# Performance work log

Hardware: AMD Instinct MI355X
Metric: run time of the kernel (lower is better)

The kernel has to match this reference:

```python
import jax, jax.numpy as jnp
import numpy as np

N_FREQ = 7  # freqs = 2**linspace(0, 6, 7) == 2**arange(7)
SKIP = (4,)


def nerf_encode(p):
    # nerfstudio NeRFEncoding with include_input=True, windows_param=None
    freqs = 2.0 ** jnp.arange(N_FREQ, dtype=p.dtype)          # [7]
    scaled = (2.0 * jnp.pi) * p                               # [N,3]
    s = (scaled[..., None] * freqs).reshape(p.shape[0], -1)   # [N,21]
    enc = jnp.sin(jnp.concatenate([s, s + 0.5 * jnp.pi], axis=-1))  # [N,42] = sin | cos
    return jnp.concatenate([enc, p], axis=-1)                 # [N,45]


def _hat_pt3d(w):
    # pytorch3d hat convention (transpose of the standard skew matrix)
    x, y, z = w[:, 0], w[:, 1], w[:, 2]
    o = jnp.zeros_like(x)
    return jnp.stack([
        jnp.stack([o, z, -y], -1),
        jnp.stack([-z, o, x], -1),
        jnp.stack([y, -x, o], -1)], -2)                       # [N,3,3]


def se3_exp_map_T(screw, eps=1e-4):
    # pytorch3d.transforms.se3_exp_map(screw).permute(0, 2, 1)
    v, w = screw[:, :3], screw[:, 3:]
    ang2 = jnp.clip(jnp.sum(w * w, axis=-1), eps, None)
    ang = jnp.sqrt(ang2)
    K = _hat_pt3d(w)
    KK = jnp.matmul(K, K)
    f1 = (jnp.sin(ang) / ang)[:, None, None]
    f2 = ((1.0 - jnp.cos(ang)) / ang2)[:, None, None]
    f3 = ((ang - jnp.sin(ang)) / (ang * ang2))[:, None, None]
    I = jnp.eye(3, dtype=screw.dtype)
    R = I + f1 * K + f2 * KK       # pytorch3d (row-vector) rotation
    V = I + f2 * K + f3 * KK
    T = jnp.einsum('nij,nj->ni', V, v)
    M = jnp.zeros((screw.shape[0], 4, 4), screw.dtype)
    M = M.at[:, :3, :3].set(jnp.swapaxes(R, -1, -2))  # transpose of [[R,0],[T,1]]
    M = M.at[:, :3, 3].set(T)
    M = M.at[:, 3, 3].set(1.0)
    return M


def mlp_stem(x, Ws, bs):
    inp = x
    n = len(Ws)
    for i in range(n):
        if i in SKIP:
            x = jnp.concatenate([inp, x], axis=-1)
        x = x @ Ws[i].T + bs[i]
        x = jax.nn.relu(x)  # hidden activation; i==n-1 is out_activation (also ReLU)
    return x


def setup_inputs() -> dict:
    key = jax.random.key(0)
    ks = jax.random.split(key, 16)
    N = 524288
    d = {
        'positions': jax.random.uniform(ks[0], (N, 3), jnp.float32),
        'directions': jax.random.normal(ks[1], (N, 3), jnp.float32),
        'warp_code': jax.random.normal(ks[2], (N, 8), jnp.float32),
    }
    fan_ins = [53, 128, 128, 128, 181, 128]
    for i, fi in enumerate(fan_ins):
        d[f'W{i}'] = jax.random.normal(ks[3 + i], (128, fi), jnp.float32) / np.sqrt(fi)
        d[f'b{i}'] = jnp.zeros((128,), jnp.float32)
    d['Wr'] = jax.random.normal(ks[10], (3, 128), jnp.float32) * 1e-5
    d['br'] = jnp.zeros((3,), jnp.float32)
    d['Wv'] = jax.random.normal(ks[11], (3, 128), jnp.float32) * 1e-5
    d['bv'] = jnp.zeros((3,), jnp.float32)
    return d


def reference(positions, directions, warp_code,
              W0, b0, W1, b1, W2, b2, W3, b3, W4, b4, W5, b5,
              Wr, br, Wv, bv):
    enc = nerf_encode(positions)                                  # [N,45]
    feat = mlp_stem(jnp.concatenate([enc, warp_code], axis=-1),
                    [W0, W1, W2, W3, W4, W5], [b0, b1, b2, b3, b4, b5])  # [N,128]
    r = feat @ Wr.T + br                                          # [N,3]
    v = feat @ Wv.T + bv                                          # [N,3]
    screw = jnp.concatenate([v, r], axis=-1)                      # [N,6]
    M = se3_exp_map_T(screw)                                      # [N,4,4]
    ph = jnp.concatenate([positions, jnp.ones_like(positions[:, :1])], axis=-1)
    wp_h = jnp.einsum('nij,nj->ni', M, ph)                        # [N,4]
    wp = wp_h[:, :3] / wp_h[:, 3:]
    wp = jnp.where(jnp.isnan(wp), positions, wp)
    rots = M[:, :3, :3]
    wd = jnp.einsum('nij,nj->ni', rots, directions)
    wd = jnp.where(jnp.isnan(wd), directions, wd)
    return wp, wd
```

## Files before the change

### kernel.cpp

```cpp
#include <hip/hip_runtime.h>
#include <hip/hip_bf16.h>
#include <math.h>


typedef __bf16 bf16x8 __attribute__((ext_vector_type(8)));
typedef float  f32x4  __attribute__((ext_vector_type(4)));

#define NROWS 524288
#define BROWS 128

#define P0 0
#define P1 8192
#define P2 24576
#define P3 40960
#define P4 57344
#define P5 81920
#define PH 98304
#define PTOT 100352

#define X0_OFF 0
#define XA_OFF 16384
#define SC_OFF 0
#define LDS_SZ 49152

template<int KS, int FAN>
__device__ __forceinline__ float pack_val(const float* __restrict__ W, int idx)
{
    int f  = idx / (KS * 512);
    int r2 = idx % (KS * 512);
    int s  = r2 >> 9, r3 = r2 & 511, ln = r3 >> 3, j = r3 & 7;
    int col = f * 16 + (ln & 15);
    int k   = s * 32 + (ln >> 4) * 8 + j;
    if (FAN == 128) return W[col * 128 + k];
    if (FAN == 53)  return (k < 53) ? W[col * 53 + k] : 0.f;
    if (k < 53)  return W[col * 181 + k];
    if (k < 64)  return 0.f;
    return W[col * 181 + (k - 11)];
}

__global__ void pack_w(const float* __restrict__ W0, const float* __restrict__ W1,
                       const float* __restrict__ W2, const float* __restrict__ W3,
                       const float* __restrict__ W4, const float* __restrict__ W5,
                       const float* __restrict__ Wr, const float* __restrict__ Wv,
                       __bf16* __restrict__ pk)
{
    int e = blockIdx.x * 256 + threadIdx.x;
    if (e >= PTOT) return;
    float val;
    if (e >= PH) {
        int rem = e - PH;
        int s = rem >> 9, r3 = rem & 511, ln = r3 >> 3, j = r3 & 7;
        int col = ln & 15;
        int k = s * 32 + (ln >> 4) * 8 + j;
        if (col < 3)      val = Wv[col * 128 + k];
        else if (col < 6) val = Wr[(col - 3) * 128 + k];
        else              val = 0.f;
    }
    else if (e < P1) val = pack_val<2, 53 >(W0, e - P0);
    else if (e < P2) val = pack_val<4, 128>(W1, e - P1);
    else if (e < P3) val = pack_val<4, 128>(W2, e - P2);
    else if (e < P4) val = pack_val<4, 128>(W3, e - P3);
    else if (e < P5) val = pack_val<6, 181>(W4, e - P4);
    else             val = pack_val<4, 128>(W5, e - P5);
    pk[e] = (__bf16)val;
}

__device__ __forceinline__ unsigned pack_bf16_2(float a, float b) {
    union { __bf16 h; unsigned short u; } x, y;
    x.h = (__bf16)a; y.h = (__bf16)b;
    return ((unsigned)y.u << 16) | (unsigned)x.u;
}

template<int KS, int SPLITS, int KSN>
__device__ __forceinline__ void mlp_layer(unsigned char* smem,
    bf16x8 (&W)[4][4], f32x4 (&Bias)[4],
    const __bf16* __restrict__ pkCur, const __bf16* __restrict__ pkNext,
    const float* __restrict__ biasNext,
    int inOff, int inStride, int outOff,
    int lane, int cl, int gp, int mfG, int nfG)
{
    f32x4 acc[4][4];
    #pragma unroll
    for (int mf = 0; mf < 4; mf++)
        #pragma unroll
        for (int nf = 0; nf < 4; nf++) acc[mf][nf] = Bias[mf];

    bf16x8 Bf[2][4];
    auto loadB = [&](bf16x8* dst, int s) {
        int base, stride, k0;
        if (s < SPLITS) { base = X0_OFF; stride = 128;      k0 = s * 32; }
        else            { base = inOff;  stride = inStride; k0 = (s - SPLITS) * 32; }
        int bc = 2 * k0 + 16 * gp;
        #pragma unroll
        for (int nf = 0; nf < 4; nf++) {
            int row = nfG * 64 + nf * 16 + cl;
            dst[nf] = *(const bf16x8*)(smem + base + row * stride
                                       + (bc ^ ((row & 7) << 4)));
        }
    };

    loadB(Bf[0], 0);
    #pragma unroll
    for (int s = 0; s < KS; s++) {
        if (s + 1 < KS) loadB(Bf[(s + 1) & 1], s + 1);
        #pragma unroll
        for (int mf = 0; mf < 4; mf++)
            #pragma unroll
            for (int nf = 0; nf < 4; nf++)
                acc[mf][nf] = __builtin_amdgcn_mfma_f32_16x16x32_bf16(
                    W[s & 3][mf], Bf[s & 1][nf], acc[mf][nf], 0, 0, 0);
        if constexpr (KS > 4) {
            if (s + 4 < KS) {
                const bf16x8* pC = (const bf16x8*)pkCur;
                #pragma unroll
                for (int mf = 0; mf < 4; mf++)
                    W[(s + 4) & 3][mf] = pC[((mfG * 4 + mf) * KS + (s + 4)) * 64 + lane];
            }
        }
    }

    __syncthreads();

    if constexpr (KSN > 0) {
        constexpr int PF = (KSN > 4) ? 4 : KSN;
        const bf16x8* pN = (const bf16x8*)pkNext;
        #pragma unroll
        for (int s = 0; s < PF; s++)
            #pragma unroll
            for (int mf = 0; mf < 4; mf++)
                W[s][mf] = pN[((mfG * 4 + mf) * KSN + s) * 64 + lane];
        #pragma unroll
        for (int mf = 0; mf < 4; mf++)
            Bias[mf] = *(const f32x4*)(biasNext + mfG * 64 + mf * 16 + gp * 4);
    }

    #pragma unroll
    for (int mf = 0; mf < 4; mf++)
        #pragma unroll
        for (int nf = 0; nf < 4; nf++) {
            int row = nfG * 64 + nf * 16 + cl;
            int bc  = 128 * mfG + 32 * mf + 8 * gp;
            f32x4 a = acc[mf][nf];
            uint2 w;
            w.x = pack_bf16_2(fmaxf(a[0], 0.f), fmaxf(a[1], 0.f));
            w.y = pack_bf16_2(fmaxf(a[2], 0.f), fmaxf(a[3], 0.f));
            *(uint2*)(smem + outOff + row * 256 + (bc ^ ((row & 7) << 4))) = w;
        }

    asm volatile("s_waitcnt lgkmcnt(0)" ::: "memory");
    __builtin_amdgcn_s_barrier();
    asm volatile("" ::: "memory");
}

__global__ __launch_bounds__(256, 3)
void se3_fused(const float* __restrict__ pos, const float* __restrict__ dir,
               const float* __restrict__ wcode,
               const float* __restrict__ b0, const float* __restrict__ b1,
               const float* __restrict__ b2, const float* __restrict__ b3,
               const float* __restrict__ b4, const float* __restrict__ b5,
               const float* __restrict__ br, const float* __restrict__ bv,
               const __bf16* __restrict__ pk,
               float* __restrict__ out)
{
    __shared__ unsigned char smem[LDS_SZ];
    const int tid  = threadIdx.x;
    const int lane = tid & 63;
    const int cl   = lane & 15;
    const int gp   = lane >> 4;
    const int wid  = tid >> 6;
    const int mfG  = wid & 1;
    const int nfG  = wid >> 1;
    const int r0   = blockIdx.x * BROWS;

    bf16x8 W[4][4];
    f32x4  Bias[4];
    {
        const bf16x8* p0v = (const bf16x8*)(pk + P0);
        #pragma unroll
        for (int s = 0; s < 2; s++)
            #pragma unroll
            for (int mf = 0; mf < 4; mf++)
                W[s][mf] = p0v[((mfG * 4 + mf) * 2 + s) * 64 + lane];
        #pragma unroll
        for (int mf = 0; mf < 4; mf++)
            Bias[mf] = *(const f32x4*)(b0 + mfG * 64 + mf * 16 + gp * 4);
    }

    {
        int row = tid >> 1, h = tid & 1;
        int g = r0 + row;
        float p0 = pos[g*3+0], p1 = pos[g*3+1], p2 = pos[g*3+2];
        float vals[32];
        if (h == 0) {
            #pragma unroll
            for (int j = 0; j < 21; j++) {
                float p = (j < 7) ? p0 : (j < 14 ? p1 : p2);
                float t = p * (float)(1 << (j % 7));
                t -= floorf(t);
                vals[j] = __sinf(6.283185307179586f * t);
            }
            #pragma unroll
            for (int j = 21; j < 32; j++) {
                int idx = j - 21;
                float p = (idx < 7) ? p0 : (idx < 14 ? p1 : p2);
                float t = p * (float)(1 << (idx % 7));
                t -= floorf(t);
                vals[j] = __cosf(6.283185307179586f * t);
            }
        } else {
            #pragma unroll
            for (int j = 0; j < 10; j++) {
                int idx = 11 + j;
                float p = (idx < 14) ? p1 : p2;
                float t = p * (float)(1 << (idx % 7));
                t -= floorf(t);
                vals[j] = __cosf(6.283185307179586f * t);
            }
            vals[10] = p0; vals[11] = p1; vals[12] = p2;
            const float4* wc4 = (const float4*)(wcode + (size_t)g * 8);
            float4 wa = wc4[0], wb = wc4[1];
            vals[13] = wa.x; vals[14] = wa.y; vals[15] = wa.z; vals[16] = wa.w;
            vals[17] = wb.x; vals[18] = wb.y; vals[19] = wb.z; vals[20] = wb.w;
            #pragma unroll
            for (int j = 21; j < 32; j++) vals[j] = 0.f;
        }
        unsigned pkd[16];
        #pragma unroll
        for (int i = 0; i < 16; i++) pkd[i] = pack_bf16_2(vals[2*i], vals[2*i+1]);
        unsigned char* base = smem + X0_OFF + row * 128;
        int sw = (row & 7) << 4;
        #pragma unroll
        for (int c = 0; c < 4; c++) {
            uint4 w; w.x = pkd[4*c]; w.y = pkd[4*c+1]; w.z = pkd[4*c+2]; w.w = pkd[4*c+3];
            *(uint4*)(base + ((64 * h + 16 * c) ^ sw)) = w;
        }
    }
    __syncthreads();

    mlp_layer<2,0,4>(smem, W, Bias, pk+P0, pk+P1, b1, X0_OFF, 128, XA_OFF, lane, cl, gp, mfG, nfG);
    mlp_layer<4,0,4>(smem, W, Bias, pk+P1, pk+P2, b2, XA_OFF, 256, XA_OFF, lane, cl, gp, mfG, nfG);
    mlp_layer<4,0,4>(smem, W, Bias, pk+P2, pk+P3, b3, XA_OFF, 256, XA_OFF, lane, cl, gp, mfG, nfG);
    mlp_layer<4,0,6>(smem, W, Bias, pk+P3, pk+P4, b4, XA_OFF, 256, XA_OFF, lane, cl, gp, mfG, nfG);
    mlp_layer<6,2,4>(smem, W, Bias, pk+P4, pk+P5, b5, XA_OFF, 256, XA_OFF, lane, cl, gp, mfG, nfG);
    mlp_layer<4,0,0>(smem, W, Bias, pk+P5, nullptr, nullptr, XA_OFF, 256, XA_OFF, lane, cl, gp, mfG, nfG);

    if (mfG == 0) {
        const bf16x8* pW = (const bf16x8*)(pk + PH);
        bf16x8 Wh[4];
        #pragma unroll
        for (int s = 0; s < 4; s++) Wh[s] = pW[s * 64 + lane];
        f32x4 hb;
        #pragma unroll
        for (int r = 0; r < 4; r++) {
            int m = gp * 4 + r;
            hb[r] = (m < 3) ? bv[m] : ((m < 6) ? br[m - 3] : 0.f);
        }
        f32x4 hacc[4];
        #pragma unroll
        for (int nf = 0; nf < 4; nf++) hacc[nf] = hb;
        #pragma unroll
        for (int s = 0; s < 4; s++) {
            int bc = 64 * s + 16 * gp;
            #pragma unroll
            for (int nf = 0; nf < 4; nf++) {
                int row = nfG * 64 + nf * 16 + cl;
                bf16x8 B = *(const bf16x8*)(smem + XA_OFF + row * 256
                                            + (bc ^ ((row & 7) << 4)));
                hacc[nf] = __builtin_amdgcn_mfma_f32_16x16x32_bf16(Wh[s], B, hacc[nf], 0, 0, 0);
            }
        }
        #pragma unroll
        for (int nf = 0; nf < 4; nf++) {
            int row = nfG * 64 + nf * 16 + cl;
            if (gp == 0) {
                *(f32x4*)(smem + SC_OFF + row * 32) = hacc[nf];
            } else if (gp == 1) {
                *(float*)(smem + SC_OFF + row * 32 + 16) = hacc[nf][0];
                *(float*)(smem + SC_OFF + row * 32 + 20) = hacc[nf][1];
            }
        }
    }
    __syncthreads();

    if (tid < BROWS) {
        int row = tid, g = r0 + row;
        const float* sc = (const float*)(smem + SC_OFF + row * 32);
        float v0 = sc[0], v1 = sc[1], v2 = sc[2];
        float wx = sc[3], wy = sc[4], wz = sc[5];
        float ang2 = wx*wx + wy*wy + wz*wz;
        ang2 = fmaxf(ang2, 1e-4f);
        float ang = sqrtf(ang2);
        float sn = __sinf(ang), cs = __cosf(ang);
        float f1 = sn / ang;
        float f2 = (1.f - cs) / ang2;
        float f3 = (ang - sn) / (ang * ang2);
        float K[3][3] = {{0.f,  wz, -wy}, {-wz, 0.f,  wx}, { wy, -wx, 0.f}};
        float KK[3][3];
        #pragma unroll
        for (int i = 0; i < 3; i++)
            #pragma unroll
            for (int j = 0; j < 3; j++)
                KK[i][j] = K[i][0]*K[0][j] + K[i][1]*K[1][j] + K[i][2]*K[2][j];
        float R[3][3], V[3][3];
        #pragma unroll
        for (int i = 0; i < 3; i++)
            #pragma unroll
            for (int j = 0; j < 3; j++) {
                float id = (i == j) ? 1.f : 0.f;
                R[i][j] = id + f1 * K[i][j] + f2 * KK[i][j];
                V[i][j] = id + f2 * K[i][j] + f3 * KK[i][j];
            }
        float T0 = V[0][0]*v0 + V[0][1]*v1 + V[0][2]*v2;
        float T1 = V[1][0]*v0 + V[1][1]*v1 + V[1][2]*v2;
        float T2 = V[2][0]*v0 + V[2][1]*v1 + V[2][2]*v2;
        float px = pos[g*3+0], py = pos[g*3+1], pz = pos[g*3+2];
        float dx = dir[g*3+0], dy = dir[g*3+1], dz = dir[g*3+2];
        float wpx = R[0][0]*px + R[1][0]*py + R[2][0]*pz + T0;
        float wpy = R[0][1]*px + R[1][1]*py + R[2][1]*pz + T1;
        float wpz = R[0][2]*px + R[1][2]*py + R[2][2]*pz + T2;
        float wdx = R[0][0]*dx + R[1][0]*dy + R[2][0]*dz;
        float wdy = R[0][1]*dx + R[1][1]*dy + R[2][1]*dz;
        float wdz = R[0][2]*dx + R[1][2]*dy + R[2][2]*dz;
        wpx = (wpx != wpx) ? px : wpx;
        wpy = (wpy != wpy) ? py : wpy;
        wpz = (wpz != wpz) ? pz : wpz;
        wdx = (wdx != wdx) ? dx : wdx;
        wdy = (wdy != wdy) ? dy : wdy;
        wdz = (wdz != wdz) ? dz : wdz;
        out[g*3+0] = wpx; out[g*3+1] = wpy; out[g*3+2] = wpz;
        float* o2 = out + (size_t)NROWS * 3;
        o2[g*3+0] = wdx; o2[g*3+1] = wdy; o2[g*3+2] = wdz;
    }
}

extern "C" void kernel_launch(void* const* d_in, const int* in_sizes, int n_in,
                              void* d_out, int out_size, void* d_ws, size_t ws_size,
                              hipStream_t stream)
{
    const float* pos = (const float*)d_in[0];
    const float* dir = (const float*)d_in[1];
    const float* wc  = (const float*)d_in[2];
    const float* W0 = (const float*)d_in[3];  const float* b0 = (const float*)d_in[4];
    const float* W1 = (const float*)d_in[5];  const float* b1 = (const float*)d_in[6];
    const float* W2 = (const float*)d_in[7];  const float* b2 = (const float*)d_in[8];
    const float* W3 = (const float*)d_in[9];  const float* b3 = (const float*)d_in[10];
    const float* W4 = (const float*)d_in[11]; const float* b4 = (const float*)d_in[12];
    const float* W5 = (const float*)d_in[13]; const float* b5 = (const float*)d_in[14];
    const float* Wr = (const float*)d_in[15]; const float* br = (const float*)d_in[16];
    const float* Wv = (const float*)d_in[17]; const float* bv = (const float*)d_in[18];
    __bf16* pk = (__bf16*)d_ws;
    float* out = (float*)d_out;

    pack_w<<<(PTOT + 255) / 256, 256, 0, stream>>>(W0, W1, W2, W3, W4, W5, Wr, Wv, pk);
    se3_fused<<<NROWS / BROWS, 256, 0, stream>>>(pos, dir, wc,
                                                 b0, b1, b2, b3, b4, b5,
                                                 br, bv, pk, out);
}
```

Baseline: 224.7 us.

## Keep MLP activations in registers and stage weights through double-buffered LDS

Each block now handles 512 rows with 8 waves. Each wave owns 64 rows and computes all 128 output features. Hidden activations stay in registers across layers and are rearranged into the next layer's B-operand layout with cross-lane shuffles, so the per-layer LDS write/read round-trip goes away. Weights and biases for the next layer are copied into a second LDS buffer with global_load_lds while the current layer runs, replacing per-wave global weight fetches into registers. The trade is about 150 KB of LDS per block, which likely limits each CU to one block, and relies on the async LDS loads being complete by the barrier.

```diff
diff --git a/kernel.cpp b/kernel.cpp
--- a/kernel.cpp
+++ b/kernel.cpp
@@ -5,9 +5,10 @@
 
 typedef __bf16 bf16x8 __attribute__((ext_vector_type(8)));
 typedef float  f32x4  __attribute__((ext_vector_type(4)));
+typedef unsigned uintx4 __attribute__((ext_vector_type(4)));
 
 #define NROWS 524288
-#define BROWS 128
+#define BROWS 512
 
 #define P0 0
 #define P1 8192
@@ -18,10 +19,12 @@
 #define PH 98304
 #define PTOT 100352
 
-#define X0_OFF 0
-#define XA_OFF 16384
-#define SC_OFF 0
-#define LDS_SZ 49152
+#define WA_OFF   0
+#define WB_OFF   49152
+#define X0_OFF   81920
+#define BIAS_OFF 147456
+#define SCREW_OFF 49152
+#define LDS_SZ   150784
 
 template<int KS, int FAN>
 __device__ __forceinline__ float pack_val(const float* __restrict__ W, int idx)
@@ -71,88 +74,88 @@
     return ((unsigned)y.u << 16) | (unsigned)x.u;
 }
 
-template<int KS, int SPLITS, int KSN>
-__device__ __forceinline__ void mlp_layer(unsigned char* smem,
-    bf16x8 (&W)[4][4], f32x4 (&Bias)[4],
-    const __bf16* __restrict__ pkCur, const __bf16* __restrict__ pkNext,
-    const float* __restrict__ biasNext,
-    int inOff, int inStride, int outOff,
-    int lane, int cl, int gp, int mfG, int nfG)
-{
-    f32x4 acc[4][4];
+__device__ __forceinline__ void gload_lds16(const __bf16* g, unsigned char* l) {
+    __builtin_amdgcn_global_load_lds(
+        (const __attribute__((address_space(1))) unsigned int*)g,
+        (__attribute__((address_space(3))) unsigned int*)l, 16, 0, 0);
+}
+
+__device__ __forceinline__ void stageW(const __bf16* __restrict__ pkL,
+                                       unsigned char* wdst, int nfrags,
+                                       int w, int lane) {
+    for (int f = w; f < nfrags; f += 8)
+        gload_lds16(pkL + f * 512 + lane * 8, wdst + f * 1024);
+}
+
+template<int KS, int SPLIT>
+__device__ __forceinline__ void layer16(
+    unsigned char* smem, int wOff, int lyr,
+    const __bf16* __restrict__ pkNext, int nFragsNext, int wOffNext,
+    uintx4 (&X)[4][4],
+    int w, int lane, int c, int g, int sA, int sB, int hiG)
+{
+    f32x4 acc[8][4];
     #pragma unroll
-    for (int mf = 0; mf < 4; mf++)
-        #pragma unroll
-        for (int nf = 0; nf < 4; nf++) acc[mf][nf] = Bias[mf];
-
-    bf16x8 Bf[2][4];
-    auto loadB = [&](bf16x8* dst, int s) {
-        int base, stride, k0;
-        if (s < SPLITS) { base = X0_OFF; stride = 128;      k0 = s * 32; }
-        else            { base = inOff;  stride = inStride; k0 = (s - SPLITS) * 32; }
-        int bc = 2 * k0 + 16 * gp;
-        #pragma unroll
-        for (int nf = 0; nf < 4; nf++) {
-            int row = nfG * 64 + nf * 16 + cl;
-            dst[nf] = *(const bf16x8*)(smem + base + row * stride
-                                       + (bc ^ ((row & 7) << 4)));
-        }
-    };
-
-    loadB(Bf[0], 0);
+    for (int mf = 0; mf < 8; mf++) {
+        f32x4 bb = *(const f32x4*)(smem + BIAS_OFF + (lyr * 128 + mf * 16 + g * 4) * 4);
+        #pragma unroll
+        for (int nf = 0; nf < 4; nf++) acc[mf][nf] = bb;
+    }
+
+    stageW(pkNext, smem + wOffNext, nFragsNext, w, lane);
+
     #pragma unroll
     for (int s = 0; s < KS; s++) {
-        if (s + 1 < KS) loadB(Bf[(s + 1) & 1], s + 1);
-        #pragma unroll
-        for (int mf = 0; mf < 4; mf++)
+        bf16x8 Bf[4];
+        #pragma unroll
+        for (int nf = 0; nf < 4; nf++) {
+            if (s < SPLIT) {
+                int row = 64 * w + nf * 16 + c;
+                Bf[nf] = *(const bf16x8*)(smem + X0_OFF + row * 128
+                                          + ((64 * s + 16 * g) ^ ((row & 7) << 4)));
+            } else {
+                Bf[nf] = __builtin_bit_cast(bf16x8, X[(s >= SPLIT) ? s - SPLIT : 0][nf]);
+            }
+        }
+        #pragma unroll
+        for (int mf = 0; mf < 8; mf++) {
+            bf16x8 Wf = *(const bf16x8*)(smem + wOff + (mf * KS + s) * 1024 + lane * 16);
             #pragma unroll
             for (int nf = 0; nf < 4; nf++)
                 acc[mf][nf] = __builtin_amdgcn_mfma_f32_16x16x32_bf16(
-                    W[s & 3][mf], Bf[s & 1][nf], acc[mf][nf], 0, 0, 0);
-        if constexpr (KS > 4) {
-            if (s + 4 < KS) {
-                const bf16x8* pC = (const bf16x8*)pkCur;
-                #pragma unroll
-                for (int mf = 0; mf < 4; mf++)
-                    W[(s + 4) & 3][mf] = pC[((mfG * 4 + mf) * KS + (s + 4)) * 64 + lane];
-            }
-        }
-    }
-
+                    Wf, Bf[nf], acc[mf][nf], 0, 0, 0);
+        }
+    }
+
+    #pragma unroll
+    for (int nf = 0; nf < 4; nf++) {
+        unsigned lo[8], hi[8];
+        #pragma unroll
+        for (int mf = 0; mf < 8; mf++) {
+            f32x4 a = acc[mf][nf];
+            lo[mf] = pack_bf16_2(fmaxf(a[0], 0.f), fmaxf(a[1], 0.f));
+            hi[mf] = pack_bf16_2(fmaxf(a[2], 0.f), fmaxf(a[3], 0.f));
+        }
+        #pragma unroll
+        for (int s = 0; s < 4; s++) {
+            unsigned e0 = (unsigned)__shfl((int)lo[2*s],   sA, 64);
+            unsigned e1 = (unsigned)__shfl((int)lo[2*s+1], sA, 64);
+            unsigned f0 = (unsigned)__shfl((int)hi[2*s],   sA, 64);
+            unsigned f1 = (unsigned)__shfl((int)hi[2*s+1], sA, 64);
+            unsigned e2 = (unsigned)__shfl((int)lo[2*s],   sB, 64);
+            unsigned e3 = (unsigned)__shfl((int)lo[2*s+1], sB, 64);
+            unsigned f2 = (unsigned)__shfl((int)hi[2*s],   sB, 64);
+            unsigned f3 = (unsigned)__shfl((int)hi[2*s+1], sB, 64);
+            X[s][nf][0] = hiG ? e1 : e0;
+            X[s][nf][1] = hiG ? f1 : f0;
+            X[s][nf][2] = hiG ? e3 : e2;
+            X[s][nf][3] = hiG ? f3 : f2;
+        }
+    }
     __syncthreads();
-
-    if constexpr (KSN > 0) {
-        constexpr int PF = (KSN > 4) ? 4 : KSN;
-        const bf16x8* pN = (const bf16x8*)pkNext;
-        #pragma unroll
-        for (int s = 0; s < PF; s++)
-            #pragma unroll
-            for (int mf = 0; mf < 4; mf++)
-                W[s][mf] = pN[((mfG * 4 + mf) * KSN + s) * 64 + lane];
-        #pragma unroll
-        for (int mf = 0; mf < 4; mf++)
-            Bias[mf] = *(const f32x4*)(biasNext + mfG * 64 + mf * 16 + gp * 4);
-    }
-
-    #pragma unroll
-    for (int mf = 0; mf < 4; mf++)
-        #pragma unroll
-        for (int nf = 0; nf < 4; nf++) {
-            int row = nfG * 64 + nf * 16 + cl;
-            int bc  = 128 * mfG + 32 * mf + 8 * gp;
-            f32x4 a = acc[mf][nf];
-            uint2 w;
-            w.x = pack_bf16_2(fmaxf(a[0], 0.f), fmaxf(a[1], 0.f));
-            w.y = pack_bf16_2(fmaxf(a[2], 0.f), fmaxf(a[3], 0.f));
-            *(uint2*)(smem + outOff + row * 256 + (bc ^ ((row & 7) << 4))) = w;
-        }
-
-    asm volatile("s_waitcnt lgkmcnt(0)" ::: "memory");
-    __builtin_amdgcn_s_barrier();
-    asm volatile("" ::: "memory");
-}
-
-__global__ __launch_bounds__(256, 3)
+}
+
+__global__ __launch_bounds__(512, 2)
 void se3_fused(const float* __restrict__ pos, const float* __restrict__ dir,
                const float* __restrict__ wcode,
                const float* __restrict__ b0, const float* __restrict__ b1,
@@ -165,126 +168,105 @@
     __shared__ unsigned char smem[LDS_SZ];
     const int tid  = threadIdx.x;
     const int lane = tid & 63;
-    const int cl   = lane & 15;
-    const int gp   = lane >> 4;
-    const int wid  = tid >> 6;
-    const int mfG  = wid & 1;
-    const int nfG  = wid >> 1;
+    const int w    = tid >> 6;
+    const int c    = lane & 15;
+    const int g    = lane >> 4;
     const int r0   = blockIdx.x * BROWS;
-
-    bf16x8 W[4][4];
-    f32x4  Bias[4];
+    const int sA   = c + 32 * (g & 1);
+    const int sB   = sA + 16;
+    const int hiG  = g >> 1;
+
+    stageW(pk + P0, smem + WA_OFF, 16, w, lane);
+
+    if (tid < 800) {
+        int l = tid >> 7, m = tid & 127;
+        float v;
+        if      (l == 0) v = b0[m];
+        else if (l == 1) v = b1[m];
+        else if (l == 2) v = b2[m];
+        else if (l == 3) v = b3[m];
+        else if (l == 4) v = b4[m];
+        else if (l == 5) v = b5[m];
+        else v = (m < 3) ? bv[m] : ((m < 6) ? br[m - 3] : 0.f);
+        *(float*)(smem + BIAS_OFF + tid * 4) = v;
+    }
+
     {
-        const bf16x8* p0v = (const bf16x8*)(pk + P0);
-        #pragma unroll
-        for (int s = 0; s < 2; s++)
-            #pragma unroll
-            for (int mf = 0; mf < 4; mf++)
-                W[s][mf] = p0v[((mfG * 4 + mf) * 2 + s) * 64 + lane];
-        #pragma unroll
-        for (int mf = 0; mf < 4; mf++)
-            Bias[mf] = *(const f32x4*)(b0 + mfG * 64 + mf * 16 + gp * 4);
-    }
+        int row = tid, gg = r0 + row;
+        float p3v[3] = { pos[gg*3+0], pos[gg*3+1], pos[gg*3+2] };
+        float vals[64];
+        #pragma unroll
+        for (int a = 0; a < 3; a++) {
+            float p = p3v[a];
+            #pragma unroll
+            for (int f = 0; f < 7; f++) {
+                float t = p * (float)(1 << f);
+                t -= floorf(t);
+                float ang = 6.283185307179586f * t;
+                vals[a*7+f]      = __sinf(ang);
+                vals[21+a*7+f]   = __cosf(ang);
+            }
+        }
+        vals[42] = p3v[0]; vals[43] = p3v[1]; vals[44] = p3v[2];
+        const float4* wc4 = (const float4*)(wcode + (size_t)gg * 8);
+        float4 wa = wc4[0], wb = wc4[1];
+        vals[45] = wa.x; vals[46] = wa.y; vals[47] = wa.z; vals[48] = wa.w;
+        vals[49] = wb.x; vals[50] = wb.y; vals[51] = wb.z; vals[52] = wb.w;
+        #pragma unroll
+        for (int q = 53; q < 64; q++) vals[q] = 0.f;
+
+        int sw = (row & 7) << 4;
+        unsigned char* base = smem + X0_OFF + row * 128;
+        #pragma unroll
+        for (int cc = 0; cc < 8; cc++) {
+            uintx4 u;
+            u[0] = pack_bf16_2(vals[cc*8+0], vals[cc*8+1]);
+            u[1] = pack_bf16_2(vals[cc*8+2], vals[cc*8+3]);
+            u[2] = pack_bf16_2(vals[cc*8+4], vals[cc*8+5]);
+            u[3] = pack_bf16_2(vals[cc*8+6], vals[cc*8+7]);
+            *(uintx4*)(base + ((16 * cc) ^ sw)) = u;
+        }
+    }
+    __syncthreads();
+
+    uintx4 X[4][4];
+    layer16<2,2>(smem, WA_OFF, 0, pk + P1, 32, WB_OFF, X, w, lane, c, g, sA, sB, hiG);
+    layer16<4,0>(smem, WB_OFF, 1, pk + P2, 32, WA_OFF, X, w, lane, c, g, sA, sB, hiG);
+    layer16<4,0>(smem, WA_OFF, 2, pk + P3, 32, WB_OFF, X, w, lane, c, g, sA, sB, hiG);
+    layer16<4,0>(smem, WB_OFF, 3, pk + P4, 48, WA_OFF, X, w, lane, c, g, sA, sB, hiG);
+    layer16<6,2>(smem, WA_OFF, 4, pk + P5, 32, WB_OFF, X, w, lane, c, g, sA, sB, hiG);
+    layer16<4,0>(smem, WB_OFF, 5, pk + PH,  4, WA_OFF, X, w, lane, c, g, sA, sB, hiG);
 
     {
-        int row = tid >> 1, h = tid & 1;
-        int g = r0 + row;
-        float p0 = pos[g*3+0], p1 = pos[g*3+1], p2 = pos[g*3+2];
-        float vals[32];
-        if (h == 0) {
-            #pragma unroll
-            for (int j = 0; j < 21; j++) {
-                float p = (j < 7) ? p0 : (j < 14 ? p1 : p2);
-                float t = p * (float)(1 << (j % 7));
-                t -= floorf(t);
-                vals[j] = __sinf(6.283185307179586f * t);
+        f32x4 hb = *(const f32x4*)(smem + BIAS_OFF + (768 + g * 4) * 4);
+        f32x4 ah[4];
+        #pragma unroll
+        for (int nf = 0; nf < 4; nf++) ah[nf] = hb;
+        #pragma unroll
+        for (int s = 0; s < 4; s++) {
+            bf16x8 Wh = *(const bf16x8*)(smem + WA_OFF + s * 1024 + lane * 16);
+            #pragma unroll
+            for (int nf = 0; nf < 4; nf++)
+                ah[nf] = __builtin_amdgcn_mfma_f32_16x16x32_bf16(
+                    Wh, __builtin_bit_cast(bf16x8, X[s][nf]), ah[nf], 0, 0, 0);
+        }
+        #pragma unroll
+        for (int nf = 0; nf < 4; nf++) {
+            int row = 64 * w + nf * 16 + c;
+            if (g == 0) {
+                *(f32x4*)(smem + SCREW_OFF + row * 32) = ah[nf];
+            } else if (g == 1) {
+                float* sp = (float*)(smem + SCREW_OFF + row * 32);
+                sp[4] = ah[nf][0];
+                sp[5] = ah[nf][1];
             }
-            #pragma unroll
-            for (int j = 21; j < 32; j++) {
-                int idx = j - 21;
-                float p = (idx < 7) ? p0 : (idx < 14 ? p1 : p2);
-                float t = p * (float)(1 << (idx % 7));
-                t -= floorf(t);
-                vals[j] = __cosf(6.283185307179586f * t);
-            }
-        } else {
-            #pragma unroll
-            for (int j = 0; j < 10; j++) {
-                int idx = 11 + j;
-                float p = (idx < 14) ? p1 : p2;
-                float t = p * (float)(1 << (idx % 7));
-                t -= floorf(t);
-                vals[j] = __cosf(6.283185307179586f * t);
-            }
-            vals[10] = p0; vals[11] = p1; vals[12] = p2;
-            const float4* wc4 = (const float4*)(wcode + (size_t)g * 8);
-            float4 wa = wc4[0], wb = wc4[1];
-            vals[13] = wa.x; vals[14] = wa.y; vals[15] = wa.z; vals[16] = wa.w;
-            vals[17] = wb.x; vals[18] = wb.y; vals[19] = wb.z; vals[20] = wb.w;
-            #pragma unroll
-            for (int j = 21; j < 32; j++) vals[j] = 0.f;
-        }
-        unsigned pkd[16];
-        #pragma unroll
-        for (int i = 0; i < 16; i++) pkd[i] = pack_bf16_2(vals[2*i], vals[2*i+1]);
-        unsigned char* base = smem + X0_OFF + row * 128;
-        int sw = (row & 7) << 4;
-        #pragma unroll
-        for (int c = 0; c < 4; c++) {
-            uint4 w; w.x = pkd[4*c]; w.y = pkd[4*c+1]; w.z = pkd[4*c+2]; w.w = pkd[4*c+3];
-            *(uint4*)(base + ((64 * h + 16 * c) ^ sw)) = w;
         }
     }
     __syncthreads();
 
-    mlp_layer<2,0,4>(smem, W, Bias, pk+P0, pk+P1, b1, X0_OFF, 128, XA_OFF, lane, cl, gp, mfG, nfG);
-    mlp_layer<4,0,4>(smem, W, Bias, pk+P1, pk+P2, b2, XA_OFF, 256, XA_OFF, lane, cl, gp, mfG, nfG);
-    mlp_layer<4,0,4>(smem, W, Bias, pk+P2, pk+P3, b3, XA_OFF, 256, XA_OFF, lane, cl, gp, mfG, nfG);
-    mlp_layer<4,0,6>(smem, W, Bias, pk+P3, pk+P4, b4, XA_OFF, 256, XA_OFF, lane, cl, gp, mfG, nfG);
-    mlp_layer<6,2,4>(smem, W, Bias, pk+P4, pk+P5, b5, XA_OFF, 256, XA_OFF, lane, cl, gp, mfG, nfG);
-    mlp_layer<4,0,0>(smem, W, Bias, pk+P5, nullptr, nullptr, XA_OFF, 256, XA_OFF, lane, cl, gp, mfG, nfG);
-
-    if (mfG == 0) {
-        const bf16x8* pW = (const bf16x8*)(pk + PH);
-        bf16x8 Wh[4];
-        #pragma unroll
-        for (int s = 0; s < 4; s++) Wh[s] = pW[s * 64 + lane];
-        f32x4 hb;
-        #pragma unroll
-        for (int r = 0; r < 4; r++) {
-            int m = gp * 4 + r;
-            hb[r] = (m < 3) ? bv[m] : ((m < 6) ? br[m - 3] : 0.f);
-        }
-        f32x4 hacc[4];
-        #pragma unroll
-        for (int nf = 0; nf < 4; nf++) hacc[nf] = hb;
-        #pragma unroll
-        for (int s = 0; s < 4; s++) {
-            int bc = 64 * s + 16 * gp;
-            #pragma unroll
-            for (int nf = 0; nf < 4; nf++) {
-                int row = nfG * 64 + nf * 16 + cl;
-                bf16x8 B = *(const bf16x8*)(smem + XA_OFF + row * 256
-                                            + (bc ^ ((row & 7) << 4)));
-                hacc[nf] = __builtin_amdgcn_mfma_f32_16x16x32_bf16(Wh[s], B, hacc[nf], 0, 0, 0);
-            }
-        }
-        #pragma unroll
-        for (int nf = 0; nf < 4; nf++) {
-            int row = nfG * 64 + nf * 16 + cl;
-            if (gp == 0) {
-                *(f32x4*)(smem + SC_OFF + row * 32) = hacc[nf];
-            } else if (gp == 1) {
-                *(float*)(smem + SC_OFF + row * 32 + 16) = hacc[nf][0];
-                *(float*)(smem + SC_OFF + row * 32 + 20) = hacc[nf][1];
-            }
-        }
-    }
-    __syncthreads();
-
-    if (tid < BROWS) {
-        int row = tid, g = r0 + row;
-        const float* sc = (const float*)(smem + SC_OFF + row * 32);
+    {
+        int row = tid, gg = r0 + row;
+        const float* sc = (const float*)(smem + SCREW_OFF + row * 32);
         float v0 = sc[0], v1 = sc[1], v2 = sc[2];
         float wx = sc[3], wy = sc[4], wz = sc[5];
         float ang2 = wx*wx + wy*wy + wz*wz;
@@ -313,8 +295,8 @@
         float T0 = V[0][0]*v0 + V[0][1]*v1 + V[0][2]*v2;
         float T1 = V[1][0]*v0 + V[1][1]*v1 + V[1][2]*v2;
         float T2 = V[2][0]*v0 + V[2][1]*v1 + V[2][2]*v2;
-        float px = pos[g*3+0], py = pos[g*3+1], pz = pos[g*3+2];
-        float dx = dir[g*3+0], dy = dir[g*3+1], dz = dir[g*3+2];
+        float px = pos[gg*3+0], py = pos[gg*3+1], pz = pos[gg*3+2];
+        float dx = dir[gg*3+0], dy = dir[gg*3+1], dz = dir[gg*3+2];
         float wpx = R[0][0]*px + R[1][0]*py + R[2][0]*pz + T0;
         float wpy = R[0][1]*px + R[1][1]*py + R[2][1]*pz + T1;
         float wpz = R[0][2]*px + R[1][2]*py + R[2][2]*pz + T2;
@@ -327,9 +309,9 @@
         wdx = (wdx != wdx) ? dx : wdx;
         wdy = (wdy != wdy) ? dy : wdy;
         wdz = (wdz != wdz) ? dz : wdz;
-        out[g*3+0] = wpx; out[g*3+1] = wpy; out[g*3+2] = wpz;
+        out[gg*3+0] = wpx; out[gg*3+1] = wpy; out[gg*3+2] = wpz;
         float* o2 = out + (size_t)NROWS * 3;
-        o2[g*3+0] = wdx; o2[g*3+1] = wdy; o2[g*3+2] = wdz;
+        o2[gg*3+0] = wdx; o2[gg*3+1] = wdy; o2[gg*3+2] = wdz;
     }
 }
 
@@ -348,11 +330,11 @@
     const float* W5 = (const float*)d_in[13]; const float* b5 = (const float*)d_in[14];
     const float* Wr = (const float*)d_in[15]; const float* br = (const float*)d_in[16];
     const float* Wv = (const float*)d_in[17]; const float* bv = (const float*)d_in[18];
-    __bf16* pk = (__bf16*)d_ws;
+    __bf16* pkb = (__bf16*)d_ws;
     float* out = (float*)d_out;
 
-    pack_w<<<(PTOT + 255) / 256, 256, 0, stream>>>(W0, W1, W2, W3, W4, W5, Wr, Wv, pk);
-    se3_fused<<<NROWS / BROWS, 256, 0, stream>>>(pos, dir, wc,
+    pack_w<<<(PTOT + 255) / 256, 256, 0, stream>>>(W0, W1, W2, W3, W4, W5, Wr, Wv, pkb);
+    se3_fused<<<NROWS / BROWS, 512, 0, stream>>>(pos, dir, wc,
                                                  b0, b1, b2, b3, b4, b5,
-                                                 br, bv, pk, out);
-}
+                                                 br, bv, pkb, out);
+}
```

Result: slower. 255.1 us (+13.5%).

## Split MLP tile across eight waves and stream weights per K-step

Applied to the files above, without the earlier changes.

The block grows from 256 to 512 threads. Each of the eight waves now computes a 32x64 output tile instead of 64x64, halving the accumulator and weight registers held per wave. Weight fragments are no longer kept resident across layers; they are streamed from global memory with a 2-deep double buffer on each K-step. All biases are staged in LDS once by the spare waves while the encoding is written. The aim is more waves per CU to hide latency, at the cost of more global weight traffic, an extra barrier per layer, and a larger LDS footprint that may limit how many blocks fit on a CU.

```diff
diff --git a/kernel.cpp b/kernel.cpp
--- a/kernel.cpp
+++ b/kernel.cpp
@@ -18,10 +18,11 @@
 #define PH 98304
 #define PTOT 100352
 
-#define X0_OFF 0
-#define XA_OFF 16384
-#define SC_OFF 0
-#define LDS_SZ 49152
+#define X0_OFF   0
+#define XA_OFF   16384
+#define BIAS_OFF 49152
+#define SC_OFF   0
+#define LDS_SZ   52352
 
 template<int KS, int FAN>
 __device__ __forceinline__ float pack_val(const float* __restrict__ W, int idx)
@@ -71,88 +72,72 @@
     return ((unsigned)y.u << 16) | (unsigned)x.u;
 }
 
-template<int KS, int SPLITS, int KSN>
+template<int KS, int SPLIT, bool BAR1>
 __device__ __forceinline__ void mlp_layer(unsigned char* smem,
-    bf16x8 (&W)[4][4], f32x4 (&Bias)[4],
-    const __bf16* __restrict__ pkCur, const __bf16* __restrict__ pkNext,
-    const float* __restrict__ biasNext,
-    int inOff, int inStride, int outOff,
-    int lane, int cl, int gp, int mfG, int nfG)
-{
-    f32x4 acc[4][4];
+    const __bf16* __restrict__ pkL, int lyr,
+    int lane, int c, int g, int mfG, int nfG)
+{
+    f32x4 acc[2][4];
     #pragma unroll
-    for (int mf = 0; mf < 4; mf++)
-        #pragma unroll
-        for (int nf = 0; nf < 4; nf++) acc[mf][nf] = Bias[mf];
-
-    bf16x8 Bf[2][4];
-    auto loadB = [&](bf16x8* dst, int s) {
-        int base, stride, k0;
-        if (s < SPLITS) { base = X0_OFF; stride = 128;      k0 = s * 32; }
-        else            { base = inOff;  stride = inStride; k0 = (s - SPLITS) * 32; }
-        int bc = 2 * k0 + 16 * gp;
-        #pragma unroll
-        for (int nf = 0; nf < 4; nf++) {
-            int row = nfG * 64 + nf * 16 + cl;
-            dst[nf] = *(const bf16x8*)(smem + base + row * stride
-                                       + (bc ^ ((row & 7) << 4)));
-        }
-    };
-
-    loadB(Bf[0], 0);
+    for (int mf = 0; mf < 2; mf++) {
+        f32x4 bb = *(const f32x4*)(smem + BIAS_OFF
+                                   + (lyr * 128 + mfG * 32 + mf * 16 + g * 4) * 4);
+        #pragma unroll
+        for (int nf = 0; nf < 4; nf++) acc[mf][nf] = bb;
+    }
+
+    const bf16x8* pW = (const bf16x8*)pkL;
+    bf16x8 Wf[2][2];
+    #pragma unroll
+    for (int mf = 0; mf < 2; mf++)
+        Wf[0][mf] = pW[((mfG * 2 + mf) * KS + 0) * 64 + lane];
+
     #pragma unroll
     for (int s = 0; s < KS; s++) {
-        if (s + 1 < KS) loadB(Bf[(s + 1) & 1], s + 1);
-        #pragma unroll
-        for (int mf = 0; mf < 4; mf++)
+        if (s + 1 < KS) {
+            #pragma unroll
+            for (int mf = 0; mf < 2; mf++)
+                Wf[(s + 1) & 1][mf] = pW[((mfG * 2 + mf) * KS + (s + 1)) * 64 + lane];
+        }
+        bf16x8 Bf[4];
+        {
+            int base, stride, k0;
+            if (s < SPLIT) { base = X0_OFF; stride = 128; k0 = s * 32; }
+            else           { base = XA_OFF; stride = 256; k0 = (s - SPLIT) * 32; }
+            int bc = 2 * k0 + 16 * g;
+            #pragma unroll
+            for (int nf = 0; nf < 4; nf++) {
+                int row = nfG * 64 + nf * 16 + c;
+                Bf[nf] = *(const bf16x8*)(smem + base + row * stride
+                                          + (bc ^ ((row & 7) << 4)));
+            }
+        }
+        #pragma unroll
+        for (int mf = 0; mf < 2; mf++)
             #pragma unroll
             for (int nf = 0; nf < 4; nf++)
                 acc[mf][nf] = __builtin_amdgcn_mfma_f32_16x16x32_bf16(
-                    W[s & 3][mf], Bf[s & 1][nf], acc[mf][nf], 0, 0, 0);
-        if constexpr (KS > 4) {
-            if (s + 4 < KS) {
-                const bf16x8* pC = (const bf16x8*)pkCur;
-                #pragma unroll
-                for (int mf = 0; mf < 4; mf++)
-                    W[(s + 4) & 3][mf] = pC[((mfG * 4 + mf) * KS + (s + 4)) * 64 + lane];
-            }
-        }
-    }
-
+                    Wf[s & 1][mf], Bf[nf], acc[mf][nf], 0, 0, 0);
+    }
+
+    if (BAR1) __syncthreads();
+
+    #pragma unroll
+    for (int mf = 0; mf < 2; mf++)
+        #pragma unroll
+        for (int nf = 0; nf < 4; nf++) {
+            int row = nfG * 64 + nf * 16 + c;
+            int bc  = 64 * mfG + 32 * mf + 8 * g;
+            f32x4 a = acc[mf][nf];
+            uint2 wv;
+            wv.x = pack_bf16_2(fmaxf(a[0], 0.f), fmaxf(a[1], 0.f));
+            wv.y = pack_bf16_2(fmaxf(a[2], 0.f), fmaxf(a[3], 0.f));
+            *(uint2*)(smem + XA_OFF + row * 256 + (bc ^ ((row & 7) << 4))) = wv;
+        }
     __syncthreads();
-
-    if constexpr (KSN > 0) {
-        constexpr int PF = (KSN > 4) ? 4 : KSN;
-        const bf16x8* pN = (const bf16x8*)pkNext;
-        #pragma unroll
-        for (int s = 0; s < PF; s++)
-            #pragma unroll
-            for (int mf = 0; mf < 4; mf++)
-                W[s][mf] = pN[((mfG * 4 + mf) * KSN + s) * 64 + lane];
-        #pragma unroll
-        for (int mf = 0; mf < 4; mf++)
-            Bias[mf] = *(const f32x4*)(biasNext + mfG * 64 + mf * 16 + gp * 4);
-    }
-
-    #pragma unroll
-    for (int mf = 0; mf < 4; mf++)
-        #pragma unroll
-        for (int nf = 0; nf < 4; nf++) {
-            int row = nfG * 64 + nf * 16 + cl;
-            int bc  = 128 * mfG + 32 * mf + 8 * gp;
-            f32x4 a = acc[mf][nf];
-            uint2 w;
-            w.x = pack_bf16_2(fmaxf(a[0], 0.f), fmaxf(a[1], 0.f));
-            w.y = pack_bf16_2(fmaxf(a[2], 0.f), fmaxf(a[3], 0.f));
-            *(uint2*)(smem + outOff + row * 256 + (bc ^ ((row & 7) << 4))) = w;
-        }
-
-    asm volatile("s_waitcnt lgkmcnt(0)" ::: "memory");
-    __builtin_amdgcn_s_barrier();
-    asm volatile("" ::: "memory");
-}
-
-__global__ __launch_bounds__(256, 3)
+}
+
+__global__ __launch_bounds__(512, 6)
 void se3_fused(const float* __restrict__ pos, const float* __restrict__ dir,
                const float* __restrict__ wcode,
                const float* __restrict__ b0, const float* __restrict__ b1,
@@ -165,31 +150,17 @@
     __shared__ unsigned char smem[LDS_SZ];
     const int tid  = threadIdx.x;
     const int lane = tid & 63;
-    const int cl   = lane & 15;
-    const int gp   = lane >> 4;
-    const int wid  = tid >> 6;
-    const int mfG  = wid & 1;
-    const int nfG  = wid >> 1;
+    const int w    = tid >> 6;
+    const int c    = lane & 15;
+    const int g    = lane >> 4;
+    const int mfG  = w & 3;
+    const int nfG  = w >> 2;
     const int r0   = blockIdx.x * BROWS;
 
-    bf16x8 W[4][4];
-    f32x4  Bias[4];
-    {
-        const bf16x8* p0v = (const bf16x8*)(pk + P0);
-        #pragma unroll
-        for (int s = 0; s < 2; s++)
-            #pragma unroll
-            for (int mf = 0; mf < 4; mf++)
-                W[s][mf] = p0v[((mfG * 4 + mf) * 2 + s) * 64 + lane];
-        #pragma unroll
-        for (int mf = 0; mf < 4; mf++)
-            Bias[mf] = *(const f32x4*)(b0 + mfG * 64 + mf * 16 + gp * 4);
-    }
-
-    {
+    if (tid < 256) {
         int row = tid >> 1, h = tid & 1;
-        int g = r0 + row;
-        float p0 = pos[g*3+0], p1 = pos[g*3+1], p2 = pos[g*3+2];
+        int gg = r0 + row;
+        float p0 = pos[gg*3+0], p1 = pos[gg*3+1], p2 = pos[gg*3+2];
         float vals[32];
         if (h == 0) {
             #pragma unroll
@@ -217,7 +188,7 @@
                 vals[j] = __cosf(6.283185307179586f * t);
             }
             vals[10] = p0; vals[11] = p1; vals[12] = p2;
-            const float4* wc4 = (const float4*)(wcode + (size_t)g * 8);
+            const float4* wc4 = (const float4*)(wcode + (size_t)gg * 8);
             float4 wa = wc4[0], wb = wc4[1];
             vals[13] = wa.x; vals[14] = wa.y; vals[15] = wa.z; vals[16] = wa.w;
             vals[17] = wb.x; vals[18] = wb.y; vals[19] = wb.z; vals[20] = wb.w;
@@ -230,60 +201,69 @@
         unsigned char* base = smem + X0_OFF + row * 128;
         int sw = (row & 7) << 4;
         #pragma unroll
-        for (int c = 0; c < 4; c++) {
-            uint4 w; w.x = pkd[4*c]; w.y = pkd[4*c+1]; w.z = pkd[4*c+2]; w.w = pkd[4*c+3];
-            *(uint4*)(base + ((64 * h + 16 * c) ^ sw)) = w;
+        for (int cc = 0; cc < 4; cc++) {
+            uint4 wv; wv.x = pkd[4*cc]; wv.y = pkd[4*cc+1];
+            wv.z = pkd[4*cc+2]; wv.w = pkd[4*cc+3];
+            *(uint4*)(base + ((64 * h + 16 * cc) ^ sw)) = wv;
+        }
+    } else {
+        for (int i = tid - 256; i < 800; i += 256) {
+            float v;
+            if (i < 768) {
+                int l = i >> 7, m = i & 127;
+                const float* bp = (l == 0) ? b0 : (l == 1) ? b1 : (l == 2) ? b2
+                               : (l == 3) ? b3 : (l == 4) ? b4 : b5;
+                v = bp[m];
+            } else {
+                int m = i - 768;
+                v = (m < 3) ? bv[m] : ((m < 6) ? br[m - 3] : 0.f);
+            }
+            *(float*)(smem + BIAS_OFF + i * 4) = v;
         }
     }
     __syncthreads();
 
-    mlp_layer<2,0,4>(smem, W, Bias, pk+P0, pk+P1, b1, X0_OFF, 128, XA_OFF, lane, cl, gp, mfG, nfG);
-    mlp_layer<4,0,4>(smem, W, Bias, pk+P1, pk+P2, b2, XA_OFF, 256, XA_OFF, lane, cl, gp, mfG, nfG);
-    mlp_layer<4,0,4>(smem, W, Bias, pk+P2, pk+P3, b3, XA_OFF, 256, XA_OFF, lane, cl, gp, mfG, nfG);
-    mlp_layer<4,0,6>(smem, W, Bias, pk+P3, pk+P4, b4, XA_OFF, 256, XA_OFF, lane, cl, gp, mfG, nfG);
-    mlp_layer<6,2,4>(smem, W, Bias, pk+P4, pk+P5, b5, XA_OFF, 256, XA_OFF, lane, cl, gp, mfG, nfG);
-    mlp_layer<4,0,0>(smem, W, Bias, pk+P5, nullptr, nullptr, XA_OFF, 256, XA_OFF, lane, cl, gp, mfG, nfG);
+    mlp_layer<2,2,false>(smem, pk + P0, 0, lane, c, g, mfG, nfG);
+    mlp_layer<4,0,true >(smem, pk + P1, 1, lane, c, g, mfG, nfG);
+    mlp_layer<4,0,true >(smem, pk + P2, 2, lane, c, g, mfG, nfG);
+    mlp_layer<4,0,true >(smem, pk + P3, 3, lane, c, g, mfG, nfG);
+    mlp_layer<6,2,true >(smem, pk + P4, 4, lane, c, g, mfG, nfG);
+    mlp_layer<4,0,true >(smem, pk + P5, 5, lane, c, g, mfG, nfG);
 
     if (mfG == 0) {
         const bf16x8* pW = (const bf16x8*)(pk + PH);
-        bf16x8 Wh[4];
-        #pragma unroll
-        for (int s = 0; s < 4; s++) Wh[s] = pW[s * 64 + lane];
-        f32x4 hb;
-        #pragma unroll
-        for (int r = 0; r < 4; r++) {
-            int m = gp * 4 + r;
-            hb[r] = (m < 3) ? bv[m] : ((m < 6) ? br[m - 3] : 0.f);
-        }
+        f32x4 hb = *(const f32x4*)(smem + BIAS_OFF + (768 + g * 4) * 4);
         f32x4 hacc[4];
         #pragma unroll
         for (int nf = 0; nf < 4; nf++) hacc[nf] = hb;
         #pragma unroll
         for (int s = 0; s < 4; s++) {
-            int bc = 64 * s + 16 * gp;
+            bf16x8 Wh = pW[s * 64 + lane];
+            int bc = 64 * s + 16 * g;
             #pragma unroll
             for (int nf = 0; nf < 4; nf++) {
-                int row = nfG * 64 + nf * 16 + cl;
+                int row = nfG * 64 + nf * 16 + c;
                 bf16x8 B = *(const bf16x8*)(smem + XA_OFF + row * 256
                                             + (bc ^ ((row & 7) << 4)));
-                hacc[nf] = __builtin_amdgcn_mfma_f32_16x16x32_bf16(Wh[s], B, hacc[nf], 0, 0, 0);
+                hacc[nf] = __builtin_amdgcn_mfma_f32_16x16x32_bf16(Wh, B, hacc[nf], 0, 0, 0);
             }
         }
         #pragma unroll
         for (int nf = 0; nf < 4; nf++) {
-            int row = nfG * 64 + nf * 16 + cl;
-            if (gp == 0) {
+            int row = nfG * 64 + nf * 16 + c;
+            if (g == 0) {
                 *(f32x4*)(smem + SC_OFF + row * 32) = hacc[nf];
-            } else if (gp == 1) {
-                *(float*)(smem + SC_OFF + row * 32 + 16) = hacc[nf][0];
-                *(float*)(smem + SC_OFF + row * 32 + 20) = hacc[nf][1];
+            } else if (g == 1) {
+                float* sp = (float*)(smem + SC_OFF + row * 32);
+                sp[4] = hacc[nf][0];
+                sp[5] = hacc[nf][1];
             }
         }
     }
     __syncthreads();
 
     if (tid < BROWS) {
-        int row = tid, g = r0 + row;
+        int row = tid, gg = r0 + row;
         const float* sc = (const float*)(smem + SC_OFF + row * 32);
         float v0 = sc[0], v1 = sc[1], v2 = sc[2];
         float wx = sc[3], wy = sc[4], wz = sc[5];
@@ -313,8 +293,8 @@
         float T0 = V[0][0]*v0 + V[0][1]*v1 + V[0][2]*v2;
         float T1 = V[1][0]*v0 + V[1][1]*v1 + V[1][2]*v2;
         float T2 = V[2][0]*v0 + V[2][1]*v1 + V[2][2]*v2;
-        float px = pos[g*3+0], py = pos[g*3+1], pz = pos[g*3+2];
-        float dx = dir[g*3+0], dy = dir[g*3+1], dz = dir[g*3+2];
+        float px = pos[gg*3+0], py = pos[gg*3+1], pz = pos[gg*3+2];
+        float dx = dir[gg*3+0], dy = dir[gg*3+1], dz = dir[gg*3+2];
         float wpx = R[0][0]*px + R[1][0]*py + R[2][0]*pz + T0;
         float wpy = R[0][1]*px + R[1][1]*py + R[2][1]*pz + T1;
         float wpz = R[0][2]*px + R[1][2]*py + R[2][2]*pz + T2;
@@ -327,9 +307,9 @@
         wdx = (wdx != wdx) ? dx : wdx;
         wdy = (wdy != wdy) ? dy : wdy;
         wdz = (wdz != wdz) ? dz : wdz;
-        out[g*3+0] = wpx; out[g*3+1] = wpy; out[g*3+2] = wpz;
+        out[gg*3+0] = wpx; out[gg*3+1] = wpy; out[gg*3+2] = wpz;
         float* o2 = out + (size_t)NROWS * 3;
-        o2[g*3+0] = wdx; o2[g*3+1] = wdy; o2[g*3+2] = wdz;
+        o2[gg*3+0] = wdx; o2[gg*3+1] = wdy; o2[gg*3+2] = wdz;
     }
 }
 
@@ -348,11 +328,11 @@
     const float* W5 = (const float*)d_in[13]; const float* b5 = (const float*)d_in[14];
     const float* Wr = (const float*)d_in[15]; const float* br = (const float*)d_in[16];
     const float* Wv = (const float*)d_in[17]; const float* bv = (const float*)d_in[18];
-    __bf16* pk = (__bf16*)d_ws;
+    __bf16* pkb = (__bf16*)d_ws;
     float* out = (float*)d_out;
 
-    pack_w<<<(PTOT + 255) / 256, 256, 0, stream>>>(W0, W1, W2, W3, W4, W5, Wr, Wv, pk);
-    se3_fused<<<NROWS / BROWS, 256, 0, stream>>>(pos, dir, wc,
+    pack_w<<<(PTOT + 255) / 256, 256, 0, stream>>>(W0, W1, W2, W3, W4, W5, Wr, Wv, pkb);
+    se3_fused<<<NROWS / BROWS, 512, 0, stream>>>(pos, dir, wc,
                                                  b0, b1, b2, b3, b4, b5,
-                                                 br, bv, pk, out);
-}
+                                                 br, bv, pkb, out);
+}
```

Result: no change. 227.1 us (+1.1%).
